# Kernel optimization log

Measured on AMD Instinct MI355X. Metric: run time of the kernel, lower is better.

The kernel has to match this reference:

```python
import jax, jax.numpy as jnp
import numpy as np

N = 4096
INPUT_DIM = 1024
H1 = 512
H2 = 256
NUM_CLASS = 16
ALPHA = 0.2  # leaky relu slope in GAT layers
NEG_INF = -9e15


def _xavier(key, shape, gain=1.414):
    fan_in, fan_out = shape[0], shape[1]
    bound = gain * np.sqrt(6.0 / (fan_in + fan_out))
    return jax.random.uniform(key, shape, jnp.float32, -bound, bound)


def setup_inputs() -> dict:
    key = jax.random.key(0)
    ks = jax.random.split(key, 16)
    X = jax.random.normal(ks[0], (N, INPUT_DIM), jnp.float32)
    Y = jax.random.normal(ks[1], (N, NUM_CLASS), jnp.float32)
    noise = jax.random.normal(ks[2], (N, H2), jnp.float32)
    adj = jax.random.bernoulli(ks[3], 32.0 / N, (N, N))  # bool mask, avg degree ~32
    # GAT layer params: W [in,out], a [2*out,1]
    W0 = _xavier(ks[4], (INPUT_DIM, H1))
    a0 = _xavier(ks[5], (2 * H1, 1))
    W1 = _xavier(ks[6], (H1 + NUM_CLASS, H2))
    a1 = _xavier(ks[7], (2 * H2, 1))
    W2 = _xavier(ks[8], (H1 + NUM_CLASS, H2))
    a2 = _xavier(ks[9], (2 * H2, 1))
    # decoder MLP
    fc1_w = _xavier(ks[10], (H2 + NUM_CLASS, H1), gain=1.0)
    fc1_b = jnp.zeros((H1,), jnp.float32)
    fc2_w = _xavier(ks[11], (H1, N), gain=1.0)
    fc2_b = jnp.zeros((N,), jnp.float32)
    return {"X": X, "Y": Y, "noise": noise, "adj": adj,
            "W0": W0, "a0": a0, "W1": W1, "a1": a1, "W2": W2, "a2": a2,
            "fc1_w": fc1_w, "fc1_b": fc1_b, "fc2_w": fc2_w, "fc2_b": fc2_b}


def gat_layer(x, W, a, adj):
    # Faithful to the torch layer but without materializing [N*N, 2F]:
    # a_input @ a == (h @ a[:F]) broadcast-added to (h @ a[F:]).T
    h = x @ W                       # [N, F]
    F_ = W.shape[1]
    f_src = (h @ a[:F_]).squeeze(-1)  # [N] contribution of row node i
    f_dst = (h @ a[F_:]).squeeze(-1)  # [N] contribution of col node j
    e = jax.nn.leaky_relu(f_src[:, None] + f_dst[None, :], ALPHA)  # [N, N]
    e = jnp.where(adj, e, NEG_INF)
    att = jax.nn.softmax(e, axis=1)  # dropout prob is 0 in this model
    h_prime = att @ h               # [N, F]
    return jax.nn.elu(h_prime)      # concat=True default -> ELU


def reference(X, Y, noise, adj, W0, a0, W1, a1, W2, a2, fc1_w, fc1_b, fc2_w, fc2_b):
    hidden = gat_layer(X, W0, a0, adj)            # [N, H1]
    hidden = jnp.concatenate([hidden, Y], axis=1)  # [N, H1+C]
    mean = gat_layer(hidden, W1, a1, adj)          # [N, H2]
    logstd = gat_layer(hidden, W2, a2, adj)        # [N, H2]
    z = noise * jnp.exp(logstd) + mean             # reparameterization
    z = jnp.concatenate([z, Y], axis=1)            # [N, H2+C]
    z = jax.nn.relu(z @ fc1_w + fc1_b)             # [N, H1]
    A_pred = jax.nn.sigmoid(z @ fc2_w + fc2_b)     # [N, N]
    return A_pred
```

## Files before the change

### kernel.cpp

```cpp
#include <hip/hip_runtime.h>

#define LRELU_ALPHA 0.2f
#define NN 4096
#define CAP 256

typedef unsigned short u16;
typedef short bf16x8 __attribute__((ext_vector_type(8)));
typedef float f32x4 __attribute__((ext_vector_type(4)));
typedef u16 u16x4 __attribute__((ext_vector_type(4)));
typedef u16 u16x2 __attribute__((ext_vector_type(2)));
typedef u16 u16x8 __attribute__((ext_vector_type(8)));

__device__ __forceinline__ u16 f2bf(float f) {
  unsigned u = __float_as_uint(f);
  u += 0x7FFFu + ((u >> 16) & 1u);
  return (u16)(u >> 16);
}
__device__ __forceinline__ float bf2f(u16 u) {
  return __uint_as_float(((unsigned)u) << 16);
}

__device__ __forceinline__ float waveSum(float v) {
  #pragma unroll
  for (int o = 32; o > 0; o >>= 1) v += __shfl_xor(v, o, 64);
  return v;
}
__device__ __forceinline__ float waveMax(float v) {
  #pragma unroll
  for (int o = 32; o > 0; o >>= 1) v = fmaxf(v, __shfl_xor(v, o, 64));
  return v;
}

__device__ __forceinline__ void gload_lds16(const void* g, void* l) {
  __builtin_amdgcn_global_load_lds((const __attribute__((address_space(1))) void*)g,
                                   (__attribute__((address_space(3))) void*)l, 16, 0, 0);
}

__device__ __forceinline__ void lds_barrier() {
  asm volatile("s_waitcnt lgkmcnt(0)" ::: "memory");
  __builtin_amdgcn_s_barrier();
}

__device__ __forceinline__ void csr_body(const unsigned* __restrict__ adjw,
                                         int* __restrict__ nbr, int* __restrict__ cnt,
                                         int i, int* scn)
{
  const int tid = threadIdx.x;
  unsigned bits = 0;
  const unsigned* row = adjw + (size_t)i * 4096 + tid * 16;
  #pragma unroll
  for (int ck = 0; ck < 4; ++ck) {
    uint4 v = *(const uint4*)(row + ck * 4);
    if (v.x) bits |= 1u << (ck * 4 + 0);
    if (v.y) bits |= 1u << (ck * 4 + 1);
    if (v.z) bits |= 1u << (ck * 4 + 2);
    if (v.w) bits |= 1u << (ck * 4 + 3);
  }
  int mycnt = __popc(bits);
  scn[tid] = mycnt;
  __syncthreads();
  for (int off = 1; off < 256; off <<= 1) {
    int v = (tid >= off) ? scn[tid - off] : 0;
    __syncthreads();
    scn[tid] += v;
    __syncthreads();
  }
  const int total = scn[255];
  int pos = scn[tid] - mycnt;
  #pragma unroll
  for (int b = 0; b < 16; ++b) {
    if (bits & (1u << b)) {
      if (pos < CAP) nbr[(size_t)i * CAP + pos] = tid * 16 + b;
      ++pos;
    }
  }
  if (tid == 0) cnt[i] = total;
}

__device__ __forceinline__ void transpose_body(const float* Wsrc, u16* Wt,
                                               int K, int N, int Kpad,
                                               int bx, int by, float (*t)[33]) {
  const int kb = by * 32, nb = bx * 32;
  const int tx = threadIdx.x & 31, ty = threadIdx.x >> 5;
  for (int i = ty; i < 32; i += 8) {
    int k = kb + i, n = nb + tx;
    t[i][tx] = (k < K && n < N) ? Wsrc[(size_t)k * N + n] : 0.f;
  }
  __syncthreads();
  for (int i = ty; i < 32; i += 8) {
    int n = nb + i, k = kb + tx;
    if (n < N && k < Kpad) Wt[(size_t)n * Kpad + k] = f2bf(t[tx][i]);
  }
}

__global__ __launch_bounds__(256) void prep_all(
    const float* __restrict__ W0, u16* __restrict__ W0t,
    const float* __restrict__ W1, u16* __restrict__ W1t,
    const float* __restrict__ W2, u16* __restrict__ W2t,
    const float* __restrict__ fc1w, u16* __restrict__ fc1t,
    const float* __restrict__ X, u16* __restrict__ Xb)
{
  __shared__ float t[32][33];
  const int i = blockIdx.x, tid = threadIdx.x;
  if (i < 512) {
    transpose_body(W0, W0t, 1024, 512, 1024, i & 15, i >> 4, t);
  } else if (i < 648) {
    int j = i - 512;
    transpose_body(W1, W1t, 528, 256, 544, j & 7, j >> 3, t);
  } else if (i < 784) {
    int j = i - 648;
    transpose_body(W2, W2t, 528, 256, 544, j & 7, j >> 3, t);
  } else if (i < 928) {
    int j = i - 784;
    transpose_body(fc1w, fc1t, 272, 512, 288, j & 15, j >> 4, t);
  } else {
    int j = i - 928;
    int idx = j * 256 + tid;
    float4 v = ((const float4*)X)[idx];
    u16x4 o = {f2bf(v.x), f2bf(v.y), f2bf(v.z), f2bf(v.w)};
    ((u16x4*)Xb)[idx] = o;
  }
}

template<int ACT, bool OBF>
__device__ __forceinline__ void gemm64_dev(
    const u16* __restrict__ A, int lda,
    const u16* __restrict__ Bt, int ldb,
    void* __restrict__ Cout, int ldc,
    int K, const float* __restrict__ bias,
    u16 (&As)[2][128 * 32], u16 (&Bs)[2][64 * 32], int bid)
{
  const int tid = threadIdx.x;
  const int lane = tid & 63, wv = tid >> 6;
  const int wm = wv >> 1, wn = wv & 1;
  const int swz = ((bid & 7) << 5) | (bid >> 3);
  const int m0 = (swz >> 3) * 128, n0 = (swz & 7) * 64;
  const int nk = K >> 5;

  f32x4 acc[4][2] = {};

  auto STAGE = [&](int buf, int kt) {
    #pragma unroll
    for (int i = 0; i < 2; ++i) {
      int c = tid + i * 256;
      int r = c >> 2;
      int s = (c & 3) ^ ((r >> 1) & 3);
      gload_lds16(A + (size_t)(m0 + r) * lda + kt * 32 + s * 8, (char*)As[buf] + (c & ~63) * 16);
    }
    {
      int c = tid;
      int r = c >> 2;
      int s = (c & 3) ^ ((r >> 1) & 3);
      gload_lds16(Bt + (size_t)(n0 + r) * ldb + kt * 32 + s * 8, (char*)Bs[buf] + (c & ~63) * 16);
    }
  };

  STAGE(0, 0);
  if (nk > 1) STAGE(1, 1);

  int cur = 0;
  for (int kt = 0; kt < nk; ++kt) {
    if (kt + 1 < nk) { asm volatile("s_waitcnt vmcnt(3)" ::: "memory"); }
    else             { asm volatile("s_waitcnt vmcnt(0)" ::: "memory"); }
    __builtin_amdgcn_s_barrier();

    bf16x8 af[4], bf_[2];
    #pragma unroll
    for (int mi = 0; mi < 4; ++mi) {
      int r = wm * 64 + mi * 16 + (lane & 15);
      int sp = (lane >> 4) ^ ((r >> 1) & 3);
      af[mi] = *(const bf16x8*)((const char*)As[cur] + r * 64 + sp * 16);
    }
    #pragma unroll
    for (int ni = 0; ni < 2; ++ni) {
      int r = wn * 32 + ni * 16 + (lane & 15);
      int sp = (lane >> 4) ^ ((r >> 1) & 3);
      bf_[ni] = *(const bf16x8*)((const char*)Bs[cur] + r * 64 + sp * 16);
    }
    __builtin_amdgcn_s_setprio(1);
    #pragma unroll
    for (int mi = 0; mi < 4; ++mi)
      #pragma unroll
      for (int ni = 0; ni < 2; ++ni)
        acc[mi][ni] = __builtin_amdgcn_mfma_f32_16x16x32_bf16(af[mi], bf_[ni], acc[mi][ni], 0, 0, 0);
    __builtin_amdgcn_s_setprio(0);

    __builtin_amdgcn_s_barrier();
    if (kt + 2 < nk) STAGE(cur, kt + 2);
    cur ^= 1;
  }

  float bv2[2];
  #pragma unroll
  for (int ni = 0; ni < 2; ++ni)
    bv2[ni] = bias ? bias[n0 + wn * 32 + ni * 16 + (lane & 15)] : 0.f;
  float* sc = (float*)As;
  #pragma unroll
  for (int mi = 0; mi < 4; ++mi) {
    lds_barrier();
    const int lr = wm * 16 + (lane >> 4) * 4;
    #pragma unroll
    for (int ni = 0; ni < 2; ++ni) {
      const int lc = wn * 32 + ni * 16 + (lane & 15);
      #pragma unroll
      for (int j = 0; j < 4; ++j) {
        float v = acc[mi][ni][j] + bv2[ni];
        if (ACT == 1) v = fmaxf(v, 0.f);
        if (ACT == 2) v = 1.f / (1.f + __expf(-v));
        sc[(lr + j) * 64 + lc] = v;
      }
    }
    lds_barrier();
    #pragma unroll
    for (int u = 0; u < 2; ++u) {
      int idx = tid + u * 256;
      int r = idx >> 4, c4 = (idx & 15) * 4;
      int grow = m0 + (r >> 4) * 64 + mi * 16 + (r & 15);
      float4 v4 = *(const float4*)(sc + r * 64 + c4);
      if (OBF) {
        u16x4 o = {f2bf(v4.x), f2bf(v4.y), f2bf(v4.z), f2bf(v4.w)};
        *(u16x4*)((u16*)Cout + (size_t)grow * ldc + n0 + c4) = o;
      } else {
        *(float4*)((float*)Cout + (size_t)grow * ldc + n0 + c4) = v4;
      }
    }
  }
}

template<int ACT, bool OBF>
__global__ __launch_bounds__(256) void gemm_mfma64(
    const u16* __restrict__ A, int lda, const u16* __restrict__ Bt, int ldb,
    void* __restrict__ Cout, int ldc, int K, const float* __restrict__ bias)
{
  __shared__ u16 As[2][128 * 32];
  __shared__ u16 Bs[2][64 * 32];
  gemm64_dev<ACT, OBF>(A, lda, Bt, ldb, Cout, ldc, K, bias, As, Bs,
                       blockIdx.y * 8 + blockIdx.x);
}

__global__ __launch_bounds__(256) void csr_gemm0(
    const u16* __restrict__ Xb, const u16* __restrict__ W0t, u16* __restrict__ h0b,
    const unsigned* __restrict__ adjw,
    int* __restrict__ nbr, int* __restrict__ cnt,
    const float* __restrict__ fc2w, u16* __restrict__ fc2t)
{
  __shared__ u16 As[2][128 * 32];
  __shared__ u16 Bs[2][64 * 32];
  if (blockIdx.x < 256) {
    gemm64_dev<0, true>(Xb, 1024, W0t, 1024, h0b, 512, 1024, nullptr, As, Bs, blockIdx.x);
  } else if (blockIdx.x < 4352) {
    csr_body(adjw, nbr, cnt, blockIdx.x - 256, (int*)As);
  } else {
    int j = blockIdx.x - 4352;
    transpose_body(fc2w, fc2t, 512, 4096, 512, j & 127, j >> 7, (float(*)[33])As);
  }
}

__global__ __launch_bounds__(512, 2) void gemm_fc2_8p(
    const u16* __restrict__ A, int lda,
    const u16* __restrict__ Bt, int ldb,
    float* __restrict__ Cout, int ldc,
    int K, const float* __restrict__ bias)
{
  __shared__ u16 As[2][2][128 * 64];
  __shared__ u16 Bs[2][2][128 * 64];
  const int tid = threadIdx.x;
  const int lane = tid & 63, wv = tid >> 6;
  const int wm = wv >> 2, wn = wv & 3;
  const int bid = blockIdx.y * 16 + blockIdx.x;
  const int swz = ((bid & 7) << 5) | (bid >> 3);
  const int m0 = (swz >> 4) * 256, n0 = (swz & 15) * 256;
  const int nk = K >> 6;

  f32x4 acc[8][4] = {};

  auto stA = [&](int slot, int h, int t) {
    const u16* Ap = A + (size_t)(m0 + h * 128) * lda + t * 64;
    #pragma unroll
    for (int i = 0; i < 2; ++i) {
      int c = tid + i * 512;
      int r = c >> 3, sl = c & 7;
      int sg = sl ^ (r & 7);
      gload_lds16(Ap + (size_t)r * lda + sg * 8, (char*)&As[slot][h][0] + (c & ~63) * 16);
    }
  };
  auto stB = [&](int slot, int h, int t) {
    const u16* Bp = Bt + (size_t)(n0 + h * 128) * ldb + t * 64;
    #pragma unroll
    for (int i = 0; i < 2; ++i) {
      int c = tid + i * 512;
      int r = c >> 3, sl = c & 7;
      int sg = sl ^ (r & 7);
      gload_lds16(Bp + (size_t)r * ldb + sg * 8, (char*)&Bs[slot][h][0] + (c & ~63) * 16);
    }
  };

  bf16x8 afl[4][2], afh[4][2], bfl[2][2], bfh[2][2];
  auto rdAq = [&](int slot, int mi0, bf16x8 (&dst)[4][2]) {
    #pragma unroll
    for (int m = 0; m < 4; ++m)
      #pragma unroll
      for (int ks = 0; ks < 2; ++ks) {
        int r = (mi0 + m) * 16 + (lane & 15);
        int sl = (ks * 4 + (lane >> 4)) ^ (r & 7);
        dst[m][ks] = *(const bf16x8*)((const char*)&As[slot][wm][0] + r * 128 + sl * 16);
      }
  };
  auto rdBq = [&](int slot, int ni0, bf16x8 (&dst)[2][2]) {
    #pragma unroll
    for (int n = 0; n < 2; ++n)
      #pragma unroll
      for (int ks = 0; ks < 2; ++ks) {
        int r = (wn & 1) * 64 + (ni0 + n) * 16 + (lane & 15);
        int sl = (ks * 4 + (lane >> 4)) ^ (r & 7);
        dst[n][ks] = *(const bf16x8*)((const char*)&Bs[slot][wn >> 1][0] + r * 128 + sl * 16);
      }
  };
  auto quad = [&](int mi0, int ni0, bf16x8 (&af)[4][2], bf16x8 (&bf)[2][2]) {
    __builtin_amdgcn_s_setprio(1);
    #pragma unroll
    for (int m = 0; m < 4; ++m)
      #pragma unroll
      for (int n = 0; n < 2; ++n)
        #pragma unroll
        for (int ks = 0; ks < 2; ++ks)
          acc[mi0 + m][ni0 + n] =
              __builtin_amdgcn_mfma_f32_16x16x32_bf16(af[m][ks], bf[n][ks], acc[mi0 + m][ni0 + n], 0, 0, 0);
    __builtin_amdgcn_s_setprio(0);
  };
  #define BARX() __builtin_amdgcn_s_barrier()

  stA(0, 0, 0); stA(0, 1, 0); stB(0, 0, 0); stB(0, 1, 0);
  stA(1, 0, 1); stA(1, 1, 1);
  asm volatile("s_waitcnt vmcnt(4)" ::: "memory");
  BARX();

  for (int j = 0; j < nk; j += 2) {
    const bool s2 = (j + 2) < nk;
    rdAq(0, 0, afl); rdBq(0, 0, bfl);
    stB(1, 0, j + 1);
    BARX(); quad(0, 0, afl, bfl); BARX();
    rdAq(0, 4, afh);
    stB(1, 1, j + 1);
    BARX(); quad(4, 0, afh, bfl); BARX();
    rdBq(0, 2, bfh);
    if (s2) stA(0, 0, j + 2);
    BARX(); quad(0, 2, afl, bfh); BARX();
    if (s2) {
      stA(0, 1, j + 2);
      asm volatile("s_waitcnt vmcnt(4)" ::: "memory");
    } else {
      asm volatile("s_waitcnt vmcnt(0)" ::: "memory");
    }
    BARX(); quad(4, 2, afh, bfh); BARX();
    rdAq(1, 0, afl); rdBq(1, 0, bfl);
    if (s2) stB(0, 0, j + 2);
    BARX(); quad(0, 0, afl, bfl); BARX();
    rdAq(1, 4, afh);
    if (s2) stB(0, 1, j + 2);
    BARX(); quad(4, 0, afh, bfl); BARX();
    rdBq(1, 2, bfh);
    if (s2) stA(1, 0, j + 3);
    BARX(); quad(0, 2, afl, bfh); BARX();
    if (s2) {
      stA(1, 1, j + 3);
      asm volatile("s_waitcnt vmcnt(4)" ::: "memory");
    } else {
      asm volatile("s_waitcnt vmcnt(0)" ::: "memory");
    }
    BARX(); quad(4, 2, afh, bfh); BARX();
  }

  float bv4[4];
  #pragma unroll
  for (int ni = 0; ni < 4; ++ni)
    bv4[ni] = bias[n0 + wn * 64 + ni * 16 + (lane & 15)];
  float* sc = (float*)As;
  #pragma unroll
  for (int mi = 0; mi < 8; ++mi) {
    lds_barrier();
    const int lr = wm * 16 + (lane >> 4) * 4;
    #pragma unroll
    for (int ni = 0; ni < 4; ++ni) {
      const int lc = wn * 64 + ni * 16 + (lane & 15);
      #pragma unroll
      for (int j = 0; j < 4; ++j) {
        float v = acc[mi][ni][j] + bv4[ni];
        v = 1.f / (1.f + __expf(-v));
        sc[(lr + j) * 256 + lc] = v;
      }
    }
    lds_barrier();
    #pragma unroll
    for (int u = 0; u < 4; ++u) {
      int idx = tid + u * 512;
      int r = idx >> 6, c4 = (idx & 63) * 4;
      int grow = m0 + (r >> 4) * 128 + mi * 16 + (r & 15);
      f32x4 v4 = *(const f32x4*)(sc + r * 256 + c4);
      __builtin_nontemporal_store(v4, (f32x4*)(Cout + (size_t)grow * ldc + n0 + c4));
    }
  }
}

__global__ __launch_bounds__(256) void fsrc_fdst_bf16(
    const u16* __restrict__ h, const float* __restrict__ a,
    float* __restrict__ fs, float* __restrict__ fd)
{
  const int wid = threadIdx.x >> 6, lane = threadIdx.x & 63;
  const int row = blockIdx.x * 4 + wid;
  u16x8 hv = *(const u16x8*)(h + (size_t)row * 512 + lane * 8);
  float s0 = 0.f, s1 = 0.f;
  #pragma unroll
  for (int j = 0; j < 8; ++j) {
    float x = bf2f(hv[j]);
    s0 = fmaf(x, a[lane * 8 + j], s0);
    s1 = fmaf(x, a[512 + lane * 8 + j], s1);
  }
  s0 = waveSum(s0);
  s1 = waveSum(s1);
  if (lane == 0) { fs[row] = s0; fd[row] = s1; }
}

__global__ __launch_bounds__(256) void fsrc_fdst12_bf16(
    const u16* __restrict__ h12,
    const float* __restrict__ a1, const float* __restrict__ a2,
    float* __restrict__ fs1, float* __restrict__ fd1,
    float* __restrict__ fs2, float* __restrict__ fd2)
{
  const int wid = threadIdx.x >> 6, lane = threadIdx.x & 63;
  const int row = blockIdx.x * 4 + wid;
  u16x8 hv = *(const u16x8*)(h12 + (size_t)row * 512 + lane * 8);
  float s0 = 0.f, s1 = 0.f;
  const bool lo = lane < 32;
  const float* av = lo ? a1 : a2;
  const int base = lo ? lane * 8 : lane * 8 - 256;
  #pragma unroll
  for (int j = 0; j < 8; ++j) {
    float x = bf2f(hv[j]);
    s0 = fmaf(x, av[base + j], s0);
    s1 = fmaf(x, av[256 + base + j], s1);
  }
  #pragma unroll
  for (int o = 16; o > 0; o >>= 1) {
    s0 += __shfl_down(s0, o, 64);
    s1 += __shfl_down(s1, o, 64);
  }
  if (lane == 0)  { fs1[row] = s0; fd1[row] = s1; }
  if (lane == 32) { fs2[row] = s0; fd2[row] = s1; }
}

__global__ __launch_bounds__(256) void agg_gat0(
    const u16* __restrict__ h,
    const float* __restrict__ fs, const float* __restrict__ fd,
    const int* __restrict__ nbr, const int* __restrict__ cnt,
    const float* __restrict__ Y, u16* __restrict__ hb)
{
  __shared__ float2 np[4][CAP];
  const int tid = threadIdx.x;
  const int w = tid >> 6, lane = tid & 63;
  const int r = blockIdx.x * 4 + w;
  int c = cnt[r]; if (c > CAP) c = CAP;
  float acc[8] = {};
  const u16* hp = h + lane * 8;

  if (c > 0) {
    const float fsi = fs[r];
    float e[4];
    int jj[4];
    #pragma unroll
    for (int k = 0; k < 4; ++k) {
      int n = lane + k * 64;
      e[k] = -3.0e38f;
      if (n < c) {
        jj[k] = nbr[(size_t)r * CAP + n];
        float v = fsi + fd[jj[k]];
        e[k] = v > 0.f ? v : LRELU_ALPHA * v;
      }
    }
    float m = waveMax(fmaxf(fmaxf(e[0], e[1]), fmaxf(e[2], e[3])));
    float p[4], ps = 0.f;
    #pragma unroll
    for (int k = 0; k < 4; ++k) {
      int n = lane + k * 64;
      p[k] = (n < c) ? __expf(e[k] - m) : 0.f;
      ps += p[k];
    }
    const float inv = 1.f / waveSum(ps);
    #pragma unroll
    for (int k = 0; k < 4; ++k) {
      int n = lane + k * 64;
      if (n < c) np[w][n] = float2{__int_as_float(jj[k]), p[k] * inv};
    }
    #pragma unroll 4
    for (int n = 0; n < c; ++n) {
      float2 e2 = np[w][n];
      int j = __float_as_int(e2.x);
      float pn = e2.y;
      u16x8 hv = *(const u16x8*)(hp + (size_t)j * 512);
      #pragma unroll
      for (int q = 0; q < 8; ++q) acc[q] = fmaf(pn, bf2f(hv[q]), acc[q]);
    }
  } else {
    for (int j = 0; j < NN; ++j) {
      u16x8 hv = *(const u16x8*)(hp + (size_t)j * 512);
      #pragma unroll
      for (int q = 0; q < 8; ++q) acc[q] += bf2f(hv[q]);
    }
    #pragma unroll
    for (int q = 0; q < 8; ++q) acc[q] *= (1.f / NN);
  }
  u16x8 o;
  #pragma unroll
  for (int q = 0; q < 8; ++q) {
    float v = acc[q] > 0.f ? acc[q] : expm1f(acc[q]);
    o[q] = f2bf(v);
  }
  u16* row = hb + (size_t)r * 544;
  *(u16x8*)(row + lane * 8) = o;
  if (lane < 4) {
    float4 yv = *(const float4*)(Y + (size_t)r * 16 + 4 * lane);
    *(u16x4*)(row + 512 + 4 * lane) = u16x4{f2bf(yv.x), f2bf(yv.y), f2bf(yv.z), f2bf(yv.w)};
  } else if (lane < 8) {
    *(u16x4*)(row + 528 + 4 * (lane - 4)) = u16x4{0, 0, 0, 0};
  }
}

__global__ __launch_bounds__(256) void agg_gat12(
    const u16* __restrict__ h12,
    const float* __restrict__ fs1, const float* __restrict__ fd1,
    const float* __restrict__ fs2, const float* __restrict__ fd2,
    const int* __restrict__ nbr, const int* __restrict__ cnt,
    const float* __restrict__ noise, const float* __restrict__ Y,
    u16* __restrict__ zcat)
{
  __shared__ float4 np[4][CAP];
  const int tid = threadIdx.x;
  const int w = tid >> 6, lane = tid & 63;
  const int r = blockIdx.x * 4 + w;
  int c = cnt[r]; if (c > CAP) c = CAP;
  float acc[8] = {};
  const u16* hp = h12 + lane * 8;

  if (c > 0) {
    const float f1 = fs1[r], f2 = fs2[r];
    float e1[4], e2[4];
    int jj[4];
    #pragma unroll
    for (int k = 0; k < 4; ++k) {
      int n = lane + k * 64;
      e1[k] = -3.0e38f; e2[k] = -3.0e38f;
      if (n < c) {
        jj[k] = nbr[(size_t)r * CAP + n];
        float v1 = f1 + fd1[jj[k]], v2 = f2 + fd2[jj[k]];
        e1[k] = v1 > 0.f ? v1 : LRELU_ALPHA * v1;
        e2[k] = v2 > 0.f ? v2 : LRELU_ALPHA * v2;
      }
    }
    float g1 = waveMax(fmaxf(fmaxf(e1[0], e1[1]), fmaxf(e1[2], e1[3])));
    float g2 = waveMax(fmaxf(fmaxf(e2[0], e2[1]), fmaxf(e2[2], e2[3])));
    float q1[4], q2[4], s1p = 0.f, s2p = 0.f;
    #pragma unroll
    for (int k = 0; k < 4; ++k) {
      int n = lane + k * 64;
      q1[k] = (n < c) ? __expf(e1[k] - g1) : 0.f;
      q2[k] = (n < c) ? __expf(e2[k] - g2) : 0.f;
      s1p += q1[k]; s2p += q2[k];
    }
    const float i1 = 1.f / waveSum(s1p);
    const float i2 = 1.f / waveSum(s2p);
    #pragma unroll
    for (int k = 0; k < 4; ++k) {
      int n = lane + k * 64;
      if (n < c) np[w][n] = float4{__int_as_float(jj[k]), q1[k] * i1, q2[k] * i2, 0.f};
    }
    const bool loHalf = (lane < 32);
    #pragma unroll 4
    for (int n = 0; n < c; ++n) {
      float4 e4 = np[w][n];
      int j = __float_as_int(e4.x);
      float pn = loHalf ? e4.y : e4.z;
      u16x8 hv = *(const u16x8*)(hp + (size_t)j * 512);
      #pragma unroll
      for (int q = 0; q < 8; ++q) acc[q] = fmaf(pn, bf2f(hv[q]), acc[q]);
    }
  } else {
    for (int j = 0; j < NN; ++j) {
      u16x8 hv = *(const u16x8*)(hp + (size_t)j * 512);
      #pragma unroll
      for (int q = 0; q < 8; ++q) acc[q] += bf2f(hv[q]);
    }
    #pragma unroll
    for (int q = 0; q < 8; ++q) acc[q] *= (1.f / NN);
  }
  float v[8];
  #pragma unroll
  for (int q = 0; q < 8; ++q) v[q] = acc[q] > 0.f ? acc[q] : expm1f(acc[q]);
  float lsd[8];
  #pragma unroll
  for (int q = 0; q < 8; ++q) lsd[q] = __shfl_xor(v[q], 32, 64);
  u16* row = zcat + (size_t)r * 288;
  if (lane < 32) {
    const float* nz = noise + (size_t)r * 256 + lane * 8;
    float4 na = *(const float4*)nz, nbv = *(const float4*)(nz + 4);
    float nzv[8] = {na.x, na.y, na.z, na.w, nbv.x, nbv.y, nbv.z, nbv.w};
    u16x8 o;
    #pragma unroll
    for (int q = 0; q < 8; ++q)
      o[q] = f2bf(fmaf(nzv[q], __expf(lsd[q]), v[q]));
    *(u16x8*)(row + lane * 8) = o;
  } else if (lane < 36) {
    float4 yv = *(const float4*)(Y + (size_t)r * 16 + 4 * (lane - 32));
    *(u16x4*)(row + 256 + 4 * (lane - 32)) = u16x4{f2bf(yv.x), f2bf(yv.y), f2bf(yv.z), f2bf(yv.w)};
  } else if (lane < 40) {
    *(u16x4*)(row + 272 + 4 * (lane - 36)) = u16x4{0, 0, 0, 0};
  }
}

extern "C" void kernel_launch(void* const* d_in, const int* in_sizes, int n_in,
                              void* d_out, int out_size, void* d_ws, size_t ws_size,
                              hipStream_t stream)
{
  const float* X     = (const float*)d_in[0];
  const float* Y     = (const float*)d_in[1];
  const float* noise = (const float*)d_in[2];
  const void*  adj   = d_in[3];
  const float* W0    = (const float*)d_in[4];
  const float* a0    = (const float*)d_in[5];
  const float* W1    = (const float*)d_in[6];
  const float* a1    = (const float*)d_in[7];
  const float* W2    = (const float*)d_in[8];
  const float* a2    = (const float*)d_in[9];
  const float* fc1w  = (const float*)d_in[10];
  const float* fc1b  = (const float*)d_in[11];
  const float* fc2w  = (const float*)d_in[12];
  const float* fc2b  = (const float*)d_in[13];
  float* out = (float*)d_out;
  char* W = (char*)d_ws;

  u16*   Xb    = (u16*)(W + 0);
  u16*   zcatb = (u16*)(W + 0);
  u16*   zzb   = (u16*)(W + 2359296);
  u16*   h0b   = (u16*)(W + 8388608);
  u16*   h12b  = (u16*)(W + 8388608);
  u16*   hb    = (u16*)(W + 16777216);
  u16*   W0t   = (u16*)(W + 21233664);
  u16*   W12t  = (u16*)(W + 22282240);
  u16*   fc1t  = (u16*)(W + 22839296);
  u16*   fc2t  = (u16*)(W + 23134208);
  int*   nbr   = (int*)(W + 27328512);
  int*   cnt   = (int*)(W + 31522816);
  float* fs0   = (float*)(W + 31539200);
  float* fd0   = fs0 + 4096;
  float* fs1   = fd0 + 4096;
  float* fd1   = fs1 + 4096;
  float* fs2   = fd1 + 4096;
  float* fd2   = fs2 + 4096;

  prep_all<<<5024, 256, 0, stream>>>(W0, W0t, W1, W12t, W2, W12t + 256 * 544,
                                     fc1w, fc1t, X, Xb);

  csr_gemm0<<<6400, 256, 0, stream>>>(Xb, W0t, h0b, (const unsigned*)adj, nbr, cnt,
                                      fc2w, fc2t);

  fsrc_fdst_bf16<<<1024, 256, 0, stream>>>(h0b, a0, fs0, fd0);
  agg_gat0<<<1024, 256, 0, stream>>>(h0b, fs0, fd0, nbr, cnt, Y, hb);

  gemm_mfma64<0, true><<<dim3(8, 32), 256, 0, stream>>>(hb, 544, W12t, 544, h12b, 512, 544, nullptr);
  fsrc_fdst12_bf16<<<1024, 256, 0, stream>>>(h12b, a1, a2, fs1, fd1, fs2, fd2);
  agg_gat12<<<1024, 256, 0, stream>>>(h12b, fs1, fd1, fs2, fd2, nbr, cnt, noise, Y, zcatb);

  gemm_mfma64<1, true><<<dim3(8, 32), 256, 0, stream>>>(zcatb, 288, fc1t, 288, zzb, 512, 288, fc1b);
  gemm_fc2_8p<<<dim3(16, 16), 512, 0, stream>>>(zzb, 512, fc2t, 512, out, 4096, 512, fc2b);
}
```

Before: 116.3 us.

## Double K-tile depth in gemm64 to 64 and widen fc2 epilogue writeback

The generic 128x64 MFMA GEMM now stages 64-wide K slices instead of 32, with an 8-way XOR swizzle, so each barrier pair covers two MFMA k-steps. To keep K a multiple of 64, the padded leading dimensions of hb, the W1/W2 transposes, zcat and fc1t are raised (544→576, 288→320), and the workspace offsets and prep grid are adjusted to match. The fc2 epilogue now stages two m-subtiles per LDS round, halving its barrier count. In exchange the kernels use more LDS, the padded K adds some extra zero work, and the larger K padding has to be zero-filled.

```diff
diff --git a/kernel.cpp b/kernel.cpp
--- a/kernel.cpp
+++ b/kernel.cpp
@@ -104,17 +104,17 @@
   const int i = blockIdx.x, tid = threadIdx.x;
   if (i < 512) {
     transpose_body(W0, W0t, 1024, 512, 1024, i & 15, i >> 4, t);
-  } else if (i < 648) {
+  } else if (i < 656) {
     int j = i - 512;
-    transpose_body(W1, W1t, 528, 256, 544, j & 7, j >> 3, t);
-  } else if (i < 784) {
-    int j = i - 648;
-    transpose_body(W2, W2t, 528, 256, 544, j & 7, j >> 3, t);
-  } else if (i < 928) {
-    int j = i - 784;
-    transpose_body(fc1w, fc1t, 272, 512, 288, j & 15, j >> 4, t);
+    transpose_body(W1, W1t, 528, 256, 576, j & 7, j >> 3, t);
+  } else if (i < 800) {
+    int j = i - 656;
+    transpose_body(W2, W2t, 528, 256, 576, j & 7, j >> 3, t);
+  } else if (i < 960) {
+    int j = i - 800;
+    transpose_body(fc1w, fc1t, 272, 512, 320, j & 15, j >> 4, t);
   } else {
-    int j = i - 928;
+    int j = i - 960;
     int idx = j * 256 + tid;
     float4 v = ((const float4*)X)[idx];
     u16x4 o = {f2bf(v.x), f2bf(v.y), f2bf(v.z), f2bf(v.w)};
@@ -128,30 +128,31 @@
     const u16* __restrict__ Bt, int ldb,
     void* __restrict__ Cout, int ldc,
     int K, const float* __restrict__ bias,
-    u16 (&As)[2][128 * 32], u16 (&Bs)[2][64 * 32], int bid)
+    u16 (&As)[2][128 * 64], u16 (&Bs)[2][64 * 64], int bid)
 {
   const int tid = threadIdx.x;
   const int lane = tid & 63, wv = tid >> 6;
   const int wm = wv >> 1, wn = wv & 1;
   const int swz = ((bid & 7) << 5) | (bid >> 3);
   const int m0 = (swz >> 3) * 128, n0 = (swz & 7) * 64;
-  const int nk = K >> 5;
+  const int nk = K >> 6;
 
   f32x4 acc[4][2] = {};
 
   auto STAGE = [&](int buf, int kt) {
+    #pragma unroll
+    for (int i = 0; i < 4; ++i) {
+      int c = tid + i * 256;
+      int r = c >> 3, sl = c & 7;
+      int sg = sl ^ (r & 7);
+      gload_lds16(A + (size_t)(m0 + r) * lda + kt * 64 + sg * 8, (char*)As[buf] + (c & ~63) * 16);
+    }
     #pragma unroll
     for (int i = 0; i < 2; ++i) {
       int c = tid + i * 256;
-      int r = c >> 2;
-      int s = (c & 3) ^ ((r >> 1) & 3);
-      gload_lds16(A + (size_t)(m0 + r) * lda + kt * 32 + s * 8, (char*)As[buf] + (c & ~63) * 16);
-    }
-    {
-      int c = tid;
-      int r = c >> 2;
-      int s = (c & 3) ^ ((r >> 1) & 3);
-      gload_lds16(Bt + (size_t)(n0 + r) * ldb + kt * 32 + s * 8, (char*)Bs[buf] + (c & ~63) * 16);
+      int r = c >> 3, sl = c & 7;
+      int sg = sl ^ (r & 7);
+      gload_lds16(Bt + (size_t)(n0 + r) * ldb + kt * 64 + sg * 8, (char*)Bs[buf] + (c & ~63) * 16);
     }
   };
 
@@ -160,30 +161,33 @@
 
   int cur = 0;
   for (int kt = 0; kt < nk; ++kt) {
-    if (kt + 1 < nk) { asm volatile("s_waitcnt vmcnt(3)" ::: "memory"); }
+    if (kt + 1 < nk) { asm volatile("s_waitcnt vmcnt(6)" ::: "memory"); }
     else             { asm volatile("s_waitcnt vmcnt(0)" ::: "memory"); }
     __builtin_amdgcn_s_barrier();
 
-    bf16x8 af[4], bf_[2];
-    #pragma unroll
-    for (int mi = 0; mi < 4; ++mi) {
-      int r = wm * 64 + mi * 16 + (lane & 15);
-      int sp = (lane >> 4) ^ ((r >> 1) & 3);
-      af[mi] = *(const bf16x8*)((const char*)As[cur] + r * 64 + sp * 16);
-    }
-    #pragma unroll
-    for (int ni = 0; ni < 2; ++ni) {
-      int r = wn * 32 + ni * 16 + (lane & 15);
-      int sp = (lane >> 4) ^ ((r >> 1) & 3);
-      bf_[ni] = *(const bf16x8*)((const char*)Bs[cur] + r * 64 + sp * 16);
-    }
-    __builtin_amdgcn_s_setprio(1);
-    #pragma unroll
-    for (int mi = 0; mi < 4; ++mi)
-      #pragma unroll
-      for (int ni = 0; ni < 2; ++ni)
-        acc[mi][ni] = __builtin_amdgcn_mfma_f32_16x16x32_bf16(af[mi], bf_[ni], acc[mi][ni], 0, 0, 0);
-    __builtin_amdgcn_s_setprio(0);
+    #pragma unroll
+    for (int ks = 0; ks < 2; ++ks) {
+      bf16x8 af[4], bf_[2];
+      #pragma unroll
+      for (int mi = 0; mi < 4; ++mi) {
+        int r = wm * 64 + mi * 16 + (lane & 15);
+        int sl = (ks * 4 + (lane >> 4)) ^ (r & 7);
+        af[mi] = *(const bf16x8*)((const char*)As[cur] + r * 128 + sl * 16);
+      }
+      #pragma unroll
+      for (int ni = 0; ni < 2; ++ni) {
+        int r = wn * 32 + ni * 16 + (lane & 15);
+        int sl = (ks * 4 + (lane >> 4)) ^ (r & 7);
+        bf_[ni] = *(const bf16x8*)((const char*)Bs[cur] + r * 128 + sl * 16);
+      }
+      __builtin_amdgcn_s_setprio(1);
+      #pragma unroll
+      for (int mi = 0; mi < 4; ++mi)
+        #pragma unroll
+        for (int ni = 0; ni < 2; ++ni)
+          acc[mi][ni] = __builtin_amdgcn_mfma_f32_16x16x32_bf16(af[mi], bf_[ni], acc[mi][ni], 0, 0, 0);
+      __builtin_amdgcn_s_setprio(0);
+    }
 
     __builtin_amdgcn_s_barrier();
     if (kt + 2 < nk) STAGE(cur, kt + 2);
@@ -232,8 +236,8 @@
     const u16* __restrict__ A, int lda, const u16* __restrict__ Bt, int ldb,
     void* __restrict__ Cout, int ldc, int K, const float* __restrict__ bias)
 {
-  __shared__ u16 As[2][128 * 32];
-  __shared__ u16 Bs[2][64 * 32];
+  __shared__ u16 As[2][128 * 64];
+  __shared__ u16 Bs[2][64 * 64];
   gemm64_dev<ACT, OBF>(A, lda, Bt, ldb, Cout, ldc, K, bias, As, Bs,
                        blockIdx.y * 8 + blockIdx.x);
 }
@@ -244,8 +248,8 @@
     int* __restrict__ nbr, int* __restrict__ cnt,
     const float* __restrict__ fc2w, u16* __restrict__ fc2t)
 {
-  __shared__ u16 As[2][128 * 32];
-  __shared__ u16 Bs[2][64 * 32];
+  __shared__ u16 As[2][128 * 64];
+  __shared__ u16 Bs[2][64 * 64];
   if (blockIdx.x < 256) {
     gemm64_dev<0, true>(Xb, 1024, W0t, 1024, h0b, 512, 1024, nullptr, As, Bs, blockIdx.x);
   } else if (blockIdx.x < 4352) {
@@ -377,25 +381,29 @@
     bv4[ni] = bias[n0 + wn * 64 + ni * 16 + (lane & 15)];
   float* sc = (float*)As;
   #pragma unroll
-  for (int mi = 0; mi < 8; ++mi) {
+  for (int mi2 = 0; mi2 < 8; mi2 += 2) {
     lds_barrier();
-    const int lr = wm * 16 + (lane >> 4) * 4;
-    #pragma unroll
-    for (int ni = 0; ni < 4; ++ni) {
-      const int lc = wn * 64 + ni * 16 + (lane & 15);
-      #pragma unroll
-      for (int j = 0; j < 4; ++j) {
-        float v = acc[mi][ni][j] + bv4[ni];
-        v = 1.f / (1.f + __expf(-v));
-        sc[(lr + j) * 256 + lc] = v;
+    #pragma unroll
+    for (int dm = 0; dm < 2; ++dm) {
+      const int mi = mi2 + dm;
+      const int lr = wm * 32 + dm * 16 + (lane >> 4) * 4;
+      #pragma unroll
+      for (int ni = 0; ni < 4; ++ni) {
+        const int lc = wn * 64 + ni * 16 + (lane & 15);
+        #pragma unroll
+        for (int j = 0; j < 4; ++j) {
+          float v = acc[mi][ni][j] + bv4[ni];
+          v = 1.f / (1.f + __expf(-v));
+          sc[(lr + j) * 256 + lc] = v;
+        }
       }
     }
     lds_barrier();
     #pragma unroll
-    for (int u = 0; u < 4; ++u) {
+    for (int u = 0; u < 8; ++u) {
       int idx = tid + u * 512;
       int r = idx >> 6, c4 = (idx & 63) * 4;
-      int grow = m0 + (r >> 4) * 128 + mi * 16 + (r & 15);
+      int grow = m0 + (r >> 5) * 128 + (mi2 + ((r >> 4) & 1)) * 16 + (r & 15);
       f32x4 v4 = *(const f32x4*)(sc + r * 256 + c4);
       __builtin_nontemporal_store(v4, (f32x4*)(Cout + (size_t)grow * ldc + n0 + c4));
     }
@@ -515,12 +523,12 @@
     float v = acc[q] > 0.f ? acc[q] : expm1f(acc[q]);
     o[q] = f2bf(v);
   }
-  u16* row = hb + (size_t)r * 544;
+  u16* row = hb + (size_t)r * 576;
   *(u16x8*)(row + lane * 8) = o;
   if (lane < 4) {
     float4 yv = *(const float4*)(Y + (size_t)r * 16 + 4 * lane);
     *(u16x4*)(row + 512 + 4 * lane) = u16x4{f2bf(yv.x), f2bf(yv.y), f2bf(yv.z), f2bf(yv.w)};
-  } else if (lane < 8) {
+  } else if (lane < 16) {
     *(u16x4*)(row + 528 + 4 * (lane - 4)) = u16x4{0, 0, 0, 0};
   }
 }
@@ -598,7 +606,7 @@
   float lsd[8];
   #pragma unroll
   for (int q = 0; q < 8; ++q) lsd[q] = __shfl_xor(v[q], 32, 64);
-  u16* row = zcat + (size_t)r * 288;
+  u16* row = zcat + (size_t)r * 320;
   if (lane < 32) {
     const float* nz = noise + (size_t)r * 256 + lane * 8;
     float4 na = *(const float4*)nz, nbv = *(const float4*)(nz + 4);
@@ -611,7 +619,7 @@
   } else if (lane < 36) {
     float4 yv = *(const float4*)(Y + (size_t)r * 16 + 4 * (lane - 32));
     *(u16x4*)(row + 256 + 4 * (lane - 32)) = u16x4{f2bf(yv.x), f2bf(yv.y), f2bf(yv.z), f2bf(yv.w)};
-  } else if (lane < 40) {
+  } else if (lane < 48) {
     *(u16x4*)(row + 272 + 4 * (lane - 36)) = u16x4{0, 0, 0, 0};
   }
 }
@@ -639,24 +647,24 @@
 
   u16*   Xb    = (u16*)(W + 0);
   u16*   zcatb = (u16*)(W + 0);
-  u16*   zzb   = (u16*)(W + 2359296);
+  u16*   zzb   = (u16*)(W + 2621440);
   u16*   h0b   = (u16*)(W + 8388608);
   u16*   h12b  = (u16*)(W + 8388608);
-  u16*   hb    = (u16*)(W + 16777216);
-  u16*   W0t   = (u16*)(W + 21233664);
-  u16*   W12t  = (u16*)(W + 22282240);
-  u16*   fc1t  = (u16*)(W + 22839296);
-  u16*   fc2t  = (u16*)(W + 23134208);
-  int*   nbr   = (int*)(W + 27328512);
-  int*   cnt   = (int*)(W + 31522816);
-  float* fs0   = (float*)(W + 31539200);
+  u16*   hb    = (u16*)(W + 12582912);
+  u16*   W0t   = (u16*)(W + 17301504);
+  u16*   W12t  = (u16*)(W + 18350080);
+  u16*   fc1t  = (u16*)(W + 18939904);
+  u16*   fc2t  = (u16*)(W + 19267584);
+  int*   nbr   = (int*)(W + 23461888);
+  int*   cnt   = (int*)(W + 27656192);
+  float* fs0   = (float*)(W + 27672576);
   float* fd0   = fs0 + 4096;
   float* fs1   = fd0 + 4096;
   float* fd1   = fs1 + 4096;
   float* fs2   = fd1 + 4096;
   float* fd2   = fs2 + 4096;
 
-  prep_all<<<5024, 256, 0, stream>>>(W0, W0t, W1, W12t, W2, W12t + 256 * 544,
+  prep_all<<<5056, 256, 0, stream>>>(W0, W0t, W1, W12t, W2, W12t + 256 * 576,
                                      fc1w, fc1t, X, Xb);
 
   csr_gemm0<<<6400, 256, 0, stream>>>(Xb, W0t, h0b, (const unsigned*)adj, nbr, cnt,
@@ -665,10 +673,10 @@
   fsrc_fdst_bf16<<<1024, 256, 0, stream>>>(h0b, a0, fs0, fd0);
   agg_gat0<<<1024, 256, 0, stream>>>(h0b, fs0, fd0, nbr, cnt, Y, hb);
 
-  gemm_mfma64<0, true><<<dim3(8, 32), 256, 0, stream>>>(hb, 544, W12t, 544, h12b, 512, 544, nullptr);
+  gemm_mfma64<0, true><<<dim3(8, 32), 256, 0, stream>>>(hb, 576, W12t, 576, h12b, 512, 576, nullptr);
   fsrc_fdst12_bf16<<<1024, 256, 0, stream>>>(h12b, a1, a2, fs1, fd1, fs2, fd2);
   agg_gat12<<<1024, 256, 0, stream>>>(h12b, fs1, fd1, fs2, fd2, nbr, cnt, noise, Y, zcatb);
 
-  gemm_mfma64<1, true><<<dim3(8, 32), 256, 0, stream>>>(zcatb, 288, fc1t, 288, zzb, 512, 288, fc1b);
+  gemm_mfma64<1, true><<<dim3(8, 32), 256, 0, stream>>>(zcatb, 320, fc1t, 320, zzb, 512, 320, fc1b);
   gemm_fc2_8p<<<dim3(16, 16), 512, 0, stream>>>(zzb, 512, fc2t, 512, out, 4096, 512, fc2b);
 }
```

New measurement: 116.0 us. About the same (-0.3%).
